# Performance work log

Hardware: AMD Instinct MI355X
Metric: run time of the kernel (lower is better)

Reference implementation:

```python
import jax, jax.numpy as jnp
import numpy as np
from jax import lax

B, T, D, H, C, FF, NH = 256, 48, 89, 128, 64, 64, 8
HD = C // NH


def _pos_encoding(n, c):
    pos = jnp.arange(n, dtype=jnp.float32)[:, None]
    div = jnp.exp(jnp.arange(0, c, 2, dtype=jnp.float32) * (-np.log(10000.0) / c))
    pe = jnp.zeros((n, c), dtype=jnp.float32)
    pe = pe.at[:, 0::2].set(jnp.sin(pos * div))
    pe = pe.at[:, 1::2].set(jnp.cos(pos * div))
    return pe


def _ln(x, g, b):
    m = x.mean(-1, keepdims=True)
    v = ((x - m) ** 2).mean(-1, keepdims=True)
    return (x - m) / jnp.sqrt(v + 1e-5) * g + b


def setup_inputs():
    key = jax.random.key(0)
    ks = iter(jax.random.split(key, 64))
    def n(shape, s=0.05):
        return (jax.random.normal(next(ks), shape) * s).astype(jnp.float32)
    x = jax.random.normal(next(ks), (B, T, D), dtype=jnp.float32)
    mask = (jax.random.uniform(next(ks), (B, T, D)) < 0.8).astype(jnp.float32)
    deltas = (jax.random.uniform(next(ks), (B, T, D)) * 5.0).astype(jnp.float32)
    last_obs = jax.random.normal(next(ks), (B, T, D), dtype=jnp.float32)
    medians = (jax.random.uniform(next(ks), (D,)) * 2.0).astype(jnp.float32)
    return dict(
        x=x, mask=mask, deltas=deltas, last_obs=last_obs, medians=medians,
        W_dh=n((H, D)), b_dh=n((H,)), W_dx=n((D, D)), b_dx=n((D,)),
        W_hist=n((D, H)), b_hist=n((D,)), W_feat=n((D, D)), b_feat=n((D,)),
        W_wc=n((D, 2 * D)), b_wc=n((D,)), W_wo=n((D, D)), b_wo=n((D,)),
        W_cls=n((1, H)), b_cls=n((1,)),
        W_ih=n((3 * H, 2 * D)), W_hh=n((3 * H, H)), b_ih=n((3 * H,)), b_hh=n((3 * H,)),
        W_inp=n((C, D)), b_inp=n((C,)), W_op1=n((H, C)), b_op1=n((H,)),
        W_op2=n((2 * T,)), b_op2=n((1,)),
        attn_in_w=n((3 * C, C)), attn_in_b=n((3 * C,)),
        attn_out_w=n((C, C)), attn_out_b=n((C,)),
        ln1_g=jnp.ones((C,)), ln1_b=jnp.zeros((C,)),
        ln2_g=jnp.ones((C,)), ln2_b=jnp.zeros((C,)),
        ff1_w=n((FF, C)), ff1_b=n((FF,)), ff2_w=n((C, FF)), ff2_b=n((C,)))


def _forward(x, mask, deltas, last_obs, medians,
             W_dh, b_dh, W_dx, b_dx, W_hist, b_hist, W_feat, b_feat,
             W_wc, b_wc, W_wo, b_wo, W_cls, b_cls,
             W_ih, W_hh, b_ih, b_hh, W_inp, b_inp, W_op1, b_op1, W_op2, b_op2,
             attn_in_w, attn_in_b, attn_out_w, attn_out_b,
             ln1_g, ln1_b, ln2_g, ln2_b, ff1_w, ff1_b, ff2_w, ff2_b):
    # Decay_obs: weight = 0.5*(1 - tanh(sign(dd)*|linear(dd)|))
    dd = deltas - medians[None, None, :]
    wd = dd @ W_wo.T + b_wo
    decay_factor = 0.5 * (1.0 - jnp.tanh(jnp.sign(dd) * jnp.abs(wd)))

    # time encoder: 1x1 conv projection + positional encoding
    pe = _pos_encoding(T, C)[None]                      # [1,T,C]
    d_lo = last_obs @ W_inp.T + b_inp + pe              # [B,T,C]
    d_df = decay_factor @ W_inp.T + b_inp + pe          # [B,T,C]
    data = jnp.concatenate([d_lo, d_df], axis=1)        # [B,2T,C]

    # torch TransformerEncoderLayer (post-norm, gelu, dropout off).
    # NOTE: layer is NOT batch_first, so attention runs over axis 0 (B);
    # axis 1 (2T) behaves as the batch — faithful to the source.
    qkv = data @ attn_in_w.T + attn_in_b                # [B,2T,3C]
    q, k, v = jnp.split(qkv, 3, axis=-1)
    q = q.reshape(B, 2 * T, NH, HD)
    k = k.reshape(B, 2 * T, NH, HD)
    v = v.reshape(B, 2 * T, NH, HD)
    scores = jnp.einsum('snhd,tnhd->nhst', q, k) / np.sqrt(HD)
    probs = jax.nn.softmax(scores, axis=-1)
    o = jnp.einsum('nhst,tnhd->snhd', probs, v).reshape(B, 2 * T, C)
    o = o @ attn_out_w.T + attn_out_b
    x1 = _ln(data + o, ln1_g, ln1_b)
    ff = jax.nn.gelu(x1 @ ff1_w.T + ff1_b, approximate=False) @ ff2_w.T + ff2_b
    data = _ln(x1 + ff, ln2_g, ln2_b)                   # [B,2T,C]

    data = data @ W_op1.T + b_op1                       # [B,2T,H]
    h0 = jnp.einsum('bnh,n->bh', data, W_op2) + b_op2[0]  # Conv1d(2T->1,k=1)

    diag_w = jnp.diagonal(W_dx)                         # temp_decay_x diag mask
    offdiag = 1.0 - jnp.eye(D, dtype=x.dtype)

    def step(carry, inp):
        h, loss = carry
        x_t, m_t, d_t = inp
        gamma_h = jnp.exp(-jax.nn.relu(d_t @ W_dh.T + b_dh))
        h = h * gamma_h
        x_h = h @ W_hist.T + b_hist
        x_r = m_t * x_t + (1.0 - m_t) * x_h
        xu = x_r @ (W_feat * offdiag).T + b_feat
        gamma_x = jnp.exp(-jax.nn.relu(d_t * diag_w + b_dx))
        beta = jnp.concatenate([gamma_x, m_t], axis=-1) @ W_wc.T + b_wc
        x_comb = beta * xu + (1.0 - beta) * x_h
        loss = loss + jnp.sum(jnp.abs(x_t - x_comb) * m_t) / (jnp.sum(m_t) + 1e-5)
        x_imp_t = m_t * x_t + (1.0 - m_t) * x_comb
        gi = jnp.concatenate([x_imp_t, m_t], axis=-1) @ W_ih.T + b_ih
        gh = h @ W_hh.T + b_hh
        ir, iz, ig = jnp.split(gi, 3, axis=-1)
        hr, hz, hg = jnp.split(gh, 3, axis=-1)
        r = jax.nn.sigmoid(ir + hr)
        z = jax.nn.sigmoid(iz + hz)
        g = jnp.tanh(ig + r * hg)
        h = (1.0 - z) * g + z * h
        return (h, loss), (x_imp_t, h)

    xs = (x.transpose(1, 0, 2), mask.transpose(1, 0, 2), deltas.transpose(1, 0, 2))
    (h, x_loss), (x_imp_T, hid_T) = lax.scan(step, (h0, jnp.zeros((), x.dtype)), xs)
    x_imp = x_imp_T.transpose(1, 0, 2)                  # [B,T,D]
    hiddens = hid_T.transpose(1, 0, 2)                  # [B,T,H]

    y_out = h @ W_cls.T + b_cls
    y_score = jax.nn.sigmoid(y_out)
    return x_imp, x_loss, hiddens, y_out, y_score


def reference(x, mask, deltas, last_obs, medians,
              W_dh, b_dh, W_dx, b_dx, W_hist, b_hist, W_feat, b_feat,
              W_wc, b_wc, W_wo, b_wo, W_cls, b_cls,
              W_ih, W_hh, b_ih, b_hh, W_inp, b_inp, W_op1, b_op1, W_op2, b_op2,
              attn_in_w, attn_in_b, attn_out_w, attn_out_b,
              ln1_g, ln1_b, ln2_g, ln2_b, ff1_w, ff1_b, ff2_w, ff2_b):
    return _forward(x, mask, deltas, last_obs, medians,
                    W_dh, b_dh, W_dx, b_dx, W_hist, b_hist, W_feat, b_feat,
                    W_wc, b_wc, W_wo, b_wo, W_cls, b_cls,
                    W_ih, W_hh, b_ih, b_hh, W_inp, b_inp, W_op1, b_op1, W_op2, b_op2,
                    attn_in_w, attn_in_b, attn_out_w, attn_out_b,
                    ln1_g, ln1_b, ln2_g, ln2_b, ff1_w, ff1_b, ff2_w, ff2_b)
```

## Files before the change

kernel.cpp:

```cpp
#include <hip/hip_runtime.h>
#include <math.h>

#define B_  256
#define T_  48
#define D_  89
#define H_  128
#define C_  64
#define NH_ 8
#define HD_ 8
#define N2T 96

#define XIMP_OFF 0
#define LOSS_OFF 1093632
#define HID_OFF  1093633
#define Y_OFF    2666497
#define YS_OFF   2666753

typedef unsigned int uint_t;
typedef _Float16 h2_t __attribute__((ext_vector_type(2)));

__device__ __forceinline__ float wave_sum64(float v) {
    v += __shfl_xor(v, 32);
    v += __shfl_xor(v, 16);
    v += __shfl_xor(v, 8);
    v += __shfl_xor(v, 4);
    v += __shfl_xor(v, 2);
    v += __shfl_xor(v, 1);
    return v;
}

__device__ __forceinline__ uint_t packh2(float lo, float hi) {
    union { h2_t h; uint_t u; } c;
    c.h.x = (_Float16)lo;
    c.h.y = (_Float16)hi;
    return c.u;
}
__device__ __forceinline__ h2_t as_h2(uint_t u) {
    union { uint_t u; h2_t h; } c;
    c.u = u;
    return c.h;
}
__device__ __forceinline__ float dot2(uint_t w, float ax, float ay, float acc) {
#if __has_builtin(__builtin_amdgcn_fdot2) && __has_builtin(__builtin_amdgcn_cvt_pkrtz)
    return __builtin_amdgcn_fdot2(as_h2(w), __builtin_amdgcn_cvt_pkrtz(ax, ay), acc, false);
#else
    h2_t h = as_h2(w);
    return fmaf((float)h.y, ay, fmaf((float)h.x, ax, acc));
#endif
}
__device__ __forceinline__ float sigm(float v) { return 1.f / (1.f + __expf(-v)); }

#define DOT96(W, A, acc) do { \
    _Pragma("unroll") \
    for (int it_ = 0; it_ < 3; ++it_) { \
        int idx_ = jj + 8 * it_; \
        uint2 w_ = ((const uint2*)(W))[idx_]; \
        float4 a_ = *(const float4*)((A) + 4 * idx_); \
        acc = dot2(w_.x, a_.x, a_.y, acc); \
        acc = dot2(w_.y, a_.z, a_.w, acc); \
    } } while (0)

#define DOT128(W, A, acc) do { \
    _Pragma("unroll") \
    for (int it_ = 0; it_ < 4; ++it_) { \
        int idx_ = jj + 8 * it_; \
        uint2 w_ = ((const uint2*)(W))[idx_]; \
        float4 a_ = *(const float4*)((A) + 4 * idx_); \
        acc = dot2(w_.x, a_.x, a_.y, acc); \
        acc = dot2(w_.y, a_.z, a_.w, acc); \
    } } while (0)

__device__ __forceinline__ void tr_f32(const float* __restrict__ s, float* __restrict__ d,
                                       int li, int R, int C) {
    int r = li / C, c = li - r * C;
    d[c * R + r] = s[li];
}

__global__ void k_prep(const float* W_wo, const float* W_inp, const float* ain_w,
                       const float* aout_w, const float* ff1_w, const float* ff2_w,
                       const float* W_op1,
                       float* W_woT, float* W_inpT, float* ain_T,
                       float* aout_T, float* ff1_T, float* ff2_T, float* op1_T) {
    int i = blockIdx.x * 256 + threadIdx.x;
    if (i < 7921)         tr_f32(W_wo,   W_woT,  i,          89, 89);
    else if (i < 13617)   tr_f32(W_inp,  W_inpT, i - 7921,   64, 89);
    else if (i < 25905)   tr_f32(ain_w,  ain_T,  i - 13617, 192, 64);
    else if (i < 30001)   tr_f32(aout_w, aout_T, i - 25905,  64, 64);
    else if (i < 34097)   tr_f32(ff1_w,  ff1_T,  i - 30001,  64, 64);
    else if (i < 38193)   tr_f32(ff2_w,  ff2_T,  i - 34097,  64, 64);
    else if (i < 46385)   tr_f32(W_op1,  op1_T,  i - 38193, 128, 64);
}

__global__ void k_pack(const float* __restrict__ W_dh, const float* __restrict__ W_hist,
                       const float* __restrict__ W_ih, const float* __restrict__ W_hh,
                       uint_t* __restrict__ wdh_h, uint_t* __restrict__ whist_h,
                       uint_t* __restrict__ wihx_h, uint_t* __restrict__ wihm_h,
                       uint_t* __restrict__ whh_h) {
    int i = blockIdx.x * 256 + threadIdx.x;
    if (i < 6144) {
        int r = i / 48, c = i - r * 48;
        const float* src = W_dh + r * 89;
        float lo = (c < 45) ? src[2 * c] : 0.f;
        float hi = (c < 44) ? src[2 * c + 1] : 0.f;
        wdh_h[i] = packh2(lo, hi);
    } else if (i < 11840) {
        int j = i - 6144;
        int r = j / 64, c = j - r * 64;
        const float* src = W_hist + r * 128;
        whist_h[j] = packh2(src[2 * c], src[2 * c + 1]);
    } else if (i < 30272) {
        int j = i - 11840;
        int r = j / 48, c = j - r * 48;
        const float* src = W_ih + (size_t)r * 178;
        float lo = (c < 45) ? src[2 * c] : 0.f;
        float hi = (c < 44) ? src[2 * c + 1] : 0.f;
        wihx_h[j] = packh2(lo, hi);
    } else if (i < 48704) {
        int j = i - 30272;
        int r = j / 48, c = j - r * 48;
        const float* src = W_ih + (size_t)r * 178 + 89;
        float lo = (c < 45) ? src[2 * c] : 0.f;
        float hi = (c < 44) ? src[2 * c + 1] : 0.f;
        wihm_h[j] = packh2(lo, hi);
    } else if (i < 73280) {
        int j = i - 48704;
        int r = j / 64, c = j - r * 64;
        const float* src = W_hh + (size_t)r * 128;
        whh_h[j] = packh2(src[2 * c], src[2 * c + 1]);
    }
}

__global__ void k_phaseA(const float* __restrict__ last_obs,
                         const float* __restrict__ deltas,
                         const float* __restrict__ medians,
                         const float* __restrict__ W_woT, const float* __restrict__ b_wo,
                         const float* __restrict__ W_inpT, const float* __restrict__ b_inp,
                         float* __restrict__ data) {
    int bt = blockIdx.x;
    int b = bt / T_;
    int t = bt - b * T_;
    __shared__ float dd[D_], lo[D_], dec[D_];
    int tid = threadIdx.x;
    int base = (b * T_ + t) * D_;
    if (tid < D_) {
        float dv = deltas[base + tid] - medians[tid];
        dd[tid] = dv;
        lo[tid] = last_obs[base + tid];
    }
    __syncthreads();
    if (tid < D_) {
        float acc = b_wo[tid];
        for (int j = 0; j < D_; ++j) acc = fmaf(dd[j], W_woT[j * D_ + tid], acc);
        float dv = dd[tid];
        float s = (dv > 0.f) ? 1.f : ((dv < 0.f) ? -1.f : 0.f);
        dec[tid] = 0.5f * (1.f - tanhf(s * fabsf(acc)));
    }
    __syncthreads();
    int c = tid & 63;
    int half = tid >> 6;
    const float* src = half ? dec : lo;
    float acc = b_inp[c];
    for (int j = 0; j < D_; ++j) acc = fmaf(src[j], W_inpT[j * C_ + c], acc);
    int i = c >> 1;
    float div = __expf((float)i * -0.28782313662425574f);
    float ang = (float)t * div;
    float pe = (c & 1) ? cosf(ang) : sinf(ang);
    data[((b * N2T) + half * T_ + t) * C_ + c] = acc + pe;
}

__global__ void k_qkv(const float* __restrict__ data,
                      const float* __restrict__ ain_T, const float* __restrict__ ain_b,
                      float* __restrict__ qb, float* __restrict__ kb, float* __restrict__ vb) {
    int bn = blockIdx.x;
    int s = bn / N2T;
    int n = bn - s * N2T;
    __shared__ float row[C_];
    int tid = threadIdx.x;
    if (tid < C_) row[tid] = data[bn * C_ + tid];
    __syncthreads();
    float acc = ain_b[tid];
    for (int j = 0; j < C_; ++j) acc = fmaf(row[j], ain_T[j * 192 + tid], acc);
    int part = tid >> 6;
    int c = tid & 63;
    int h = c >> 3, d = c & 7;
    float* dst = (part == 0) ? qb : ((part == 1) ? kb : vb);
    dst[(((n * NH_ + h) * B_ + s) * HD_) + d] = acc;
}

__global__ void k_attn(const float* __restrict__ qb, const float* __restrict__ kb,
                       const float* __restrict__ vb, float* __restrict__ attnO) {
    int n = blockIdx.x >> 3;
    int h = blockIdx.x & 7;
    __shared__ float k_lds[B_][HD_ + 1];
    __shared__ float v_lds[B_][HD_ + 1];
    int s = threadIdx.x;
    const float scale = 0.35355339059327373f;
    size_t base = ((size_t)blockIdx.x * B_ + s) * HD_;
    float q[HD_];
    #pragma unroll
    for (int d = 0; d < HD_; ++d) q[d] = qb[base + d] * scale;
    #pragma unroll
    for (int d = 0; d < HD_; ++d) { k_lds[s][d] = kb[base + d]; v_lds[s][d] = vb[base + d]; }
    __syncthreads();
    float m = -1e30f;
    for (int t = 0; t < B_; ++t) {
        float sc = 0.f;
        #pragma unroll
        for (int d = 0; d < HD_; ++d) sc = fmaf(q[d], k_lds[t][d], sc);
        m = fmaxf(m, sc);
    }
    float l = 0.f;
    float acc[HD_] = {0.f, 0.f, 0.f, 0.f, 0.f, 0.f, 0.f, 0.f};
    for (int t = 0; t < B_; ++t) {
        float sc = 0.f;
        #pragma unroll
        for (int d = 0; d < HD_; ++d) sc = fmaf(q[d], k_lds[t][d], sc);
        float p = __expf(sc - m);
        l += p;
        #pragma unroll
        for (int d = 0; d < HD_; ++d) acc[d] = fmaf(p, v_lds[t][d], acc[d]);
    }
    float inv = 1.f / l;
    float* op = attnO + ((size_t)s * N2T + n) * C_ + h * HD_;
    #pragma unroll
    for (int d = 0; d < HD_; ++d) op[d] = acc[d] * inv;
}

__global__ void k_transform(const float* __restrict__ data,
                            const float* __restrict__ attnO,
                            const float* __restrict__ aout_T, const float* __restrict__ aout_b,
                            const float* __restrict__ ln1_g, const float* __restrict__ ln1_b,
                            const float* __restrict__ ff1_T, const float* __restrict__ ff1_b,
                            const float* __restrict__ ff2_T, const float* __restrict__ ff2_b,
                            const float* __restrict__ ln2_g, const float* __restrict__ ln2_b,
                            const float* __restrict__ op1_T, const float* __restrict__ b_op1,
                            float* __restrict__ val) {
    int bn = blockIdx.x;
    __shared__ float orow[C_], x1s[C_], hbuf[C_], x2s[C_];
    int c = threadIdx.x;
    float d0 = data[bn * C_ + c];
    orow[c] = attnO[bn * C_ + c];
    __syncthreads();
    float acc = aout_b[c];
    for (int j = 0; j < C_; ++j) acc = fmaf(orow[j], aout_T[j * C_ + c], acc);
    float r = d0 + acc;
    float mean = wave_sum64(r) * (1.f / 64.f);
    float df = r - mean;
    float var = wave_sum64(df * df) * (1.f / 64.f);
    float x1 = df * rsqrtf(var + 1e-5f) * ln1_g[c] + ln1_b[c];
    x1s[c] = x1;
    __syncthreads();
    acc = ff1_b[c];
    for (int j = 0; j < C_; ++j) acc = fmaf(x1s[j], ff1_T[j * C_ + c], acc);
    float ge = 0.5f * acc * (1.f + erff(acc * 0.7071067811865475f));
    hbuf[c] = ge;
    __syncthreads();
    acc = ff2_b[c];
    for (int j = 0; j < C_; ++j) acc = fmaf(hbuf[j], ff2_T[j * C_ + c], acc);
    float r2 = x1 + acc;
    float mean2 = wave_sum64(r2) * (1.f / 64.f);
    float df2 = r2 - mean2;
    float var2 = wave_sum64(df2 * df2) * (1.f / 64.f);
    float x2 = df2 * rsqrtf(var2 + 1e-5f) * ln2_g[c] + ln2_b[c];
    x2s[c] = x2;
    __syncthreads();
    #pragma unroll
    for (int rep = 0; rep < 2; ++rep) {
        int k = c + rep * 64;
        float a2 = b_op1[k];
        for (int j = 0; j < C_; ++j) a2 = fmaf(x2s[j], op1_T[j * H_ + k], a2);
        val[(size_t)bn * H_ + k] = a2;
    }
}

__global__ void k_reduce_h0(const float* __restrict__ val,
                            const float* __restrict__ W_op2, const float* __restrict__ b_op2,
                            float* __restrict__ h0) {
    int b = blockIdx.x;
    int h = threadIdx.x;
    float acc = b_op2[0];
    for (int n = 0; n < N2T; ++n)
        acc = fmaf(val[((size_t)b * N2T + n) * H_ + h], W_op2[n], acc);
    h0[b * H_ + h] = acc;
}

__global__ void k_den(const float* __restrict__ mask, float* __restrict__ den) {
    int t = blockIdx.x;
    int tid = threadIdx.x;
    float s = 0.f;
    const int total = B_ * D_;
    for (int i = tid; i < total; i += 256) {
        int b = i / D_;
        int d = i - b * D_;
        s += mask[(b * T_ + t) * D_ + d];
    }
    s = wave_sum64(s);
    __shared__ float red[4];
    if ((tid & 63) == 0) red[tid >> 6] = s;
    __syncthreads();
    if (tid == 0) den[t] = red[0] + red[1] + red[2] + red[3];
}

__global__ __launch_bounds__(1024)
void k_scan(const float* __restrict__ x, const float* __restrict__ mask,
            const float* __restrict__ deltas,
            const uint_t* __restrict__ wdh_h, const float* __restrict__ b_dh,
            const float* __restrict__ W_dx, const float* __restrict__ b_dx,
            const uint_t* __restrict__ whist_h, const float* __restrict__ b_hist,
            const float* __restrict__ W_feat, const float* __restrict__ b_feat,
            const float* __restrict__ W_wc, const float* __restrict__ b_wc,
            const uint_t* __restrict__ wihx_h, const uint_t* __restrict__ wihm_h,
            const uint_t* __restrict__ whh_h,
            const float* __restrict__ b_ih, const float* __restrict__ b_hh,
            const float* __restrict__ W_cls, const float* __restrict__ b_cls,
            const float* __restrict__ h0,
            float* __restrict__ out, float* __restrict__ num_part) {
    int b = blockIdx.x;
    int tid = threadIdx.x;
    int wave = tid >> 6;
    int lane = tid & 63;
    int oo = lane >> 3;
    int jj = lane & 7;

    __shared__ __align__(16) float h_s[H_];
    __shared__ __align__(16) float xt_s[96], dt_s[96], xr_s[96], xh_s[96];
    __shared__ __align__(16) float m_s[96], gx_s[96], ximp_s[96], beta_s[96], diff_s[96];
    __shared__ __align__(16) float gis[384], ghs[384];
    __shared__ __align__(16) uint_t wwcg_l[89 * 48];
    __shared__ __align__(16) uint_t wwcm_l[89 * 48];
    __shared__ __align__(16) uint_t wfeat_l[89 * 48];

    float dxw = 0.f, dxb = 0.f;
    if (tid >= 320 && tid < 409) {
        int o = tid - 320;
        dxw = W_dx[o * 90];
        dxb = b_dx[o];
    }

    for (int i = tid; i < 89 * 48; i += 1024) {
        int r = i / 48, c = i - r * 48;
        const float* wr = W_wc + (size_t)r * 178;
        float lo = (c < 45) ? wr[2 * c] : 0.f;
        float hi = (c < 44) ? wr[2 * c + 1] : 0.f;
        wwcg_l[i] = packh2(lo, hi);
        const float* wm = wr + 89;
        float lo2 = (c < 45) ? wm[2 * c] : 0.f;
        float hi2 = (c < 44) ? wm[2 * c + 1] : 0.f;
        wwcm_l[i] = packh2(lo2, hi2);
        const float* wf = W_feat + r * 89;
        float lo3 = (c < 45 && 2 * c != r) ? wf[2 * c] : 0.f;
        float hi3 = (c < 44 && 2 * c + 1 != r) ? wf[2 * c + 1] : 0.f;
        wfeat_l[i] = packh2(lo3, hi3);
    }
    if (tid < 128) h_s[tid] = h0[b * H_ + tid];
    if (tid >= 416 && tid < 423) {
        int l = tid - 416;
        dt_s[89 + l] = 0.f; xr_s[89 + l] = 0.f; m_s[89 + l] = 0.f;
        gx_s[89 + l] = 0.f; ximp_s[89 + l] = 0.f;
    }
    {
        int base = b * T_ * D_;
        if (tid >= 128 && tid < 217) xt_s[tid - 128] = x[base + tid - 128];
        else if (tid >= 224 && tid < 313) m_s[tid - 224] = mask[base + tid - 224];
        else if (tid >= 320 && tid < 409) {
            int o = tid - 320;
            float dv = deltas[base + o];
            dt_s[o] = dv;
            gx_s[o] = __expf(-fmaxf(dv * dxw + dxb, 0.f));
        }
    }
    __syncthreads();

    for (int t = 0; t < T_; ++t) {
        for (int c = wave; c < 76; c += 16) {
            if (c < 16) {
                int o = c * 8 + oo;
                float acc = 0.f;
                DOT96(wdh_h + o * 48, dt_s, acc);
                acc += __shfl_xor(acc, 1); acc += __shfl_xor(acc, 2); acc += __shfl_xor(acc, 4);
                if (jj == 0) h_s[o] *= __expf(-fmaxf(acc + b_dh[o], 0.f));
            } else if (c < 28) {
                int o = (c - 16) * 8 + oo;
                int ro = (o < 89) ? o : 88;
                float acc = 0.f;
                DOT96(wwcg_l + ro * 48, gx_s, acc);
                DOT96(wwcm_l + ro * 48, m_s, acc);
                acc += __shfl_xor(acc, 1); acc += __shfl_xor(acc, 2); acc += __shfl_xor(acc, 4);
                if (jj == 0 && o < 89) beta_s[o] = acc + b_wc[o];
            } else {
                int o = (c - 28) * 8 + oo;
                float acc = 0.f;
                DOT96(wihm_h + o * 48, m_s, acc);
                acc += __shfl_xor(acc, 1); acc += __shfl_xor(acc, 2); acc += __shfl_xor(acc, 4);
                if (jj == 0) gis[o] = acc + b_ih[o];
            }
        }
        __syncthreads();
        for (int c = wave; c < 60; c += 16) {
            if (c < 12) {
                int o = c * 8 + oo;
                int ro = (o < 89) ? o : 88;
                float acc = 0.f;
                DOT128(whist_h + ro * 64, h_s, acc);
                acc += __shfl_xor(acc, 1); acc += __shfl_xor(acc, 2); acc += __shfl_xor(acc, 4);
                if (jj == 0 && o < 89) {
                    float xh = acc + b_hist[o];
                    xh_s[o] = xh;
                    float m = m_s[o];
                    xr_s[o] = m * xt_s[o] + (1.f - m) * xh;
                }
            } else {
                int o = (c - 12) * 8 + oo;
                float acc = 0.f;
                DOT128(whh_h + o * 64, h_s, acc);
                acc += __shfl_xor(acc, 1); acc += __shfl_xor(acc, 2); acc += __shfl_xor(acc, 4);
                if (jj == 0) ghs[o] = acc + b_hh[o];
            }
        }
        __syncthreads();
        for (int c = wave; c < 12; c += 16) {
            int o = c * 8 + oo;
            int ro = (o < 89) ? o : 88;
            float xu = 0.f;
            DOT96(wfeat_l + ro * 48, xr_s, xu);
            xu += __shfl_xor(xu, 1); xu += __shfl_xor(xu, 2); xu += __shfl_xor(xu, 4);
            if (jj == 0 && o < 89) {
                float xuf = xu + b_feat[o];
                float btf = beta_s[o];
                float xc = btf * xuf + (1.f - btf) * xh_s[o];
                float m = m_s[o];
                float xtv = xt_s[o];
                float xi = m * xtv + (1.f - m) * xc;
                ximp_s[o] = xi;
                out[XIMP_OFF + (b * T_ + t) * D_ + o] = xi;
                diff_s[o] = fabsf(xtv - xc) * m;
            }
        }
        __syncthreads();
        for (int c = wave; c < 48; c += 16) {
            int o = c * 8 + oo;
            float acc = 0.f;
            DOT96(wihx_h + o * 48, ximp_s, acc);
            acc += __shfl_xor(acc, 1); acc += __shfl_xor(acc, 2); acc += __shfl_xor(acc, 4);
            if (jj == 0) gis[o] += acc;
        }
        __syncthreads();
        if (tid < 128) {
            float r = sigm(gis[tid] + ghs[tid]);
            float z = sigm(gis[128 + tid] + ghs[128 + tid]);
            float g = tanhf(gis[256 + tid] + r * ghs[256 + tid]);
            float hn = (1.f - z) * g + z * h_s[tid];
            h_s[tid] = hn;
            out[HID_OFF + (size_t)(b * T_ + t) * H_ + tid] = hn;
        } else if (tid >= 960) {
            int l = tid - 960;
            float s = diff_s[l] + ((l < 25) ? diff_s[64 + l] : 0.f);
            s = wave_sum64(s);
            if (l == 0) num_part[t * B_ + b] = s;
        } else if (t + 1 < T_) {
            int nb = (b * T_ + t + 1) * D_;
            if (tid < 217) xt_s[tid - 128] = x[nb + tid - 128];
            else if (tid >= 224 && tid < 313) m_s[tid - 224] = mask[nb + tid - 224];
            else if (tid >= 320 && tid < 409) {
                int o = tid - 320;
                float dv = deltas[nb + o];
                dt_s[o] = dv;
                gx_s[o] = __expf(-fmaxf(dv * dxw + dxb, 0.f));
            }
        }
        __syncthreads();
    }
    if (tid < 64) {
        float p = h_s[tid] * W_cls[tid] + h_s[tid + 64] * W_cls[tid + 64];
        p = wave_sum64(p);
        if (tid == 0) {
            float y = p + b_cls[0];
            out[Y_OFF + b] = y;
            out[YS_OFF + b] = 1.f / (1.f + __expf(-y));
        }
    }
}

__global__ void k_loss(const float* __restrict__ num_part, const float* __restrict__ den,
                       float* __restrict__ out) {
    int tid = threadIdx.x;
    float v = 0.f;
    if (tid < T_) {
        float s = 0.f;
        const float* np_ = num_part + tid * B_;
        for (int b = 0; b < B_; ++b) s += np_[b];
        v = s / (den[tid] + 1e-5f);
    }
    v = wave_sum64(v);
    if (tid == 0) out[LOSS_OFF] = v;
}

extern "C" void kernel_launch(void* const* d_in, const int* in_sizes, int n_in,
                              void* d_out, int out_size, void* d_ws, size_t ws_size,
                              hipStream_t stream) {
    const float* x        = (const float*)d_in[0];
    const float* mask     = (const float*)d_in[1];
    const float* deltas   = (const float*)d_in[2];
    const float* last_obs = (const float*)d_in[3];
    const float* medians  = (const float*)d_in[4];
    const float* W_dh  = (const float*)d_in[5];
    const float* b_dh  = (const float*)d_in[6];
    const float* W_dx  = (const float*)d_in[7];
    const float* b_dx  = (const float*)d_in[8];
    const float* W_hist= (const float*)d_in[9];
    const float* b_hist= (const float*)d_in[10];
    const float* W_feat= (const float*)d_in[11];
    const float* b_feat= (const float*)d_in[12];
    const float* W_wc  = (const float*)d_in[13];
    const float* b_wc  = (const float*)d_in[14];
    const float* W_wo  = (const float*)d_in[15];
    const float* b_wo  = (const float*)d_in[16];
    const float* W_cls = (const float*)d_in[17];
    const float* b_cls = (const float*)d_in[18];
    const float* W_ih  = (const float*)d_in[19];
    const float* W_hh  = (const float*)d_in[20];
    const float* b_ih  = (const float*)d_in[21];
    const float* b_hh  = (const float*)d_in[22];
    const float* W_inp = (const float*)d_in[23];
    const float* b_inp = (const float*)d_in[24];
    const float* W_op1 = (const float*)d_in[25];
    const float* b_op1 = (const float*)d_in[26];
    const float* W_op2 = (const float*)d_in[27];
    const float* b_op2 = (const float*)d_in[28];
    const float* attn_in_w  = (const float*)d_in[29];
    const float* attn_in_b  = (const float*)d_in[30];
    const float* attn_out_w = (const float*)d_in[31];
    const float* attn_out_b = (const float*)d_in[32];
    const float* ln1_g = (const float*)d_in[33];
    const float* ln1_b = (const float*)d_in[34];
    const float* ln2_g = (const float*)d_in[35];
    const float* ln2_b = (const float*)d_in[36];
    const float* ff1_w = (const float*)d_in[37];
    const float* ff1_b = (const float*)d_in[38];
    const float* ff2_w = (const float*)d_in[39];
    const float* ff2_b = (const float*)d_in[40];

    float* out = (float*)d_out;
    float* ws = (float*)d_ws;

    float* data  = ws;
    float* qb    = data  + (size_t)B_ * N2T * C_;
    float* kb    = qb    + (size_t)N2T * NH_ * B_ * HD_;
    float* vb    = kb    + (size_t)N2T * NH_ * B_ * HD_;
    float* attnO = vb    + (size_t)N2T * NH_ * B_ * HD_;
    float* val   = attnO + (size_t)B_ * N2T * C_;
    float* h0    = val   + (size_t)B_ * N2T * H_;
    float* den   = h0    + (size_t)B_ * H_;
    float* nump  = den   + 64;
    float* W_woT = nump  + T_ * B_;
    float* W_inpT= W_woT + 7921;
    float* ain_T = W_inpT + 5696;
    float* aout_T= ain_T + 12288;
    float* ff1_T = aout_T + 4096;
    float* ff2_T = ff1_T + 4096;
    float* op1_T = ff2_T + 4096;
    uint_t* wdh_h   = (uint_t*)(op1_T + 8192);
    uint_t* whist_h = wdh_h + 6144;
    uint_t* wihx_h  = whist_h + 5696;
    uint_t* wihm_h  = wihx_h + 18432;
    uint_t* whh_h   = wihm_h + 18432;

    k_prep<<<182, 256, 0, stream>>>(W_wo, W_inp, attn_in_w, attn_out_w, ff1_w, ff2_w, W_op1,
                                    W_woT, W_inpT, ain_T, aout_T, ff1_T, ff2_T, op1_T);
    k_pack<<<287, 256, 0, stream>>>(W_dh, W_hist, W_ih, W_hh,
                                    wdh_h, whist_h, wihx_h, wihm_h, whh_h);
    k_phaseA<<<B_ * T_, 128, 0, stream>>>(last_obs, deltas, medians, W_woT, b_wo, W_inpT, b_inp, data);
    k_qkv<<<B_ * N2T, 192, 0, stream>>>(data, ain_T, attn_in_b, qb, kb, vb);
    k_attn<<<N2T * NH_, 256, 0, stream>>>(qb, kb, vb, attnO);
    k_transform<<<B_ * N2T, 64, 0, stream>>>(data, attnO, aout_T, attn_out_b,
                                             ln1_g, ln1_b, ff1_T, ff1_b, ff2_T, ff2_b,
                                             ln2_g, ln2_b, op1_T, b_op1, val);
    k_reduce_h0<<<B_, H_, 0, stream>>>(val, W_op2, b_op2, h0);
    k_den<<<T_, 256, 0, stream>>>(mask, den);
    k_scan<<<B_, 1024, 0, stream>>>(x, mask, deltas,
                                    wdh_h, b_dh, W_dx, b_dx, whist_h, b_hist, W_feat, b_feat,
                                    W_wc, b_wc, wihx_h, wihm_h, whh_h, b_ih, b_hh, W_cls, b_cls,
                                    h0, out, nump);
    k_loss<<<1, 64, 0, stream>>>(nump, den, out);
}
```

Measured before the change: 591.8 us.

## Fuse QKV into attention, merge weight prep kernels, pack scan activations to fp16

```diff
diff --git a/kernel.cpp b/kernel.cpp
--- a/kernel.cpp
+++ b/kernel.cpp
@@ -40,34 +40,34 @@
     c.u = u;
     return c.h;
 }
-__device__ __forceinline__ float dot2(uint_t w, float ax, float ay, float acc) {
-#if __has_builtin(__builtin_amdgcn_fdot2) && __has_builtin(__builtin_amdgcn_cvt_pkrtz)
-    return __builtin_amdgcn_fdot2(as_h2(w), __builtin_amdgcn_cvt_pkrtz(ax, ay), acc, false);
+__device__ __forceinline__ float dot2h(uint_t w, uint_t a, float acc) {
+#if __has_builtin(__builtin_amdgcn_fdot2)
+    return __builtin_amdgcn_fdot2(as_h2(w), as_h2(a), acc, false);
 #else
-    h2_t h = as_h2(w);
-    return fmaf((float)h.y, ay, fmaf((float)h.x, ax, acc));
+    h2_t hw = as_h2(w), ha = as_h2(a);
+    return fmaf((float)hw.y, (float)ha.y, fmaf((float)hw.x, (float)ha.x, acc));
 #endif
 }
 __device__ __forceinline__ float sigm(float v) { return 1.f / (1.f + __expf(-v)); }
 
-#define DOT96(W, A, acc) do { \
+#define DOT96H(W, A, acc) do { \
     _Pragma("unroll") \
     for (int it_ = 0; it_ < 3; ++it_) { \
         int idx_ = jj + 8 * it_; \
         uint2 w_ = ((const uint2*)(W))[idx_]; \
-        float4 a_ = *(const float4*)((A) + 4 * idx_); \
-        acc = dot2(w_.x, a_.x, a_.y, acc); \
-        acc = dot2(w_.y, a_.z, a_.w, acc); \
+        uint2 a_ = ((const uint2*)(A))[idx_]; \
+        acc = dot2h(w_.x, a_.x, acc); \
+        acc = dot2h(w_.y, a_.y, acc); \
     } } while (0)
 
-#define DOT128(W, A, acc) do { \
+#define DOT128H(W, A, acc) do { \
     _Pragma("unroll") \
     for (int it_ = 0; it_ < 4; ++it_) { \
         int idx_ = jj + 8 * it_; \
         uint2 w_ = ((const uint2*)(W))[idx_]; \
-        float4 a_ = *(const float4*)((A) + 4 * idx_); \
-        acc = dot2(w_.x, a_.x, a_.y, acc); \
-        acc = dot2(w_.y, a_.z, a_.w, acc); \
+        uint2 a_ = ((const uint2*)(A))[idx_]; \
+        acc = dot2h(w_.x, a_.x, acc); \
+        acc = dot2h(w_.y, a_.y, acc); \
     } } while (0)
 
 __device__ __forceinline__ void tr_f32(const float* __restrict__ s, float* __restrict__ d,
@@ -76,11 +76,16 @@
     d[c * R + r] = s[li];
 }
 
-__global__ void k_prep(const float* W_wo, const float* W_inp, const float* ain_w,
-                       const float* aout_w, const float* ff1_w, const float* ff2_w,
-                       const float* W_op1,
-                       float* W_woT, float* W_inpT, float* ain_T,
-                       float* aout_T, float* ff1_T, float* ff2_T, float* op1_T) {
+__global__ void k_wprep(const float* W_wo, const float* W_inp, const float* ain_w,
+                        const float* aout_w, const float* ff1_w, const float* ff2_w,
+                        const float* W_op1,
+                        float* W_woT, float* W_inpT, float* ain_T,
+                        float* aout_T, float* ff1_T, float* ff2_T, float* op1_T,
+                        const float* __restrict__ W_dh, const float* __restrict__ W_hist,
+                        const float* __restrict__ W_ih, const float* __restrict__ W_hh,
+                        uint_t* __restrict__ wdh_h, uint_t* __restrict__ whist_h,
+                        uint_t* __restrict__ wihx_h, uint_t* __restrict__ wihm_h,
+                        uint_t* __restrict__ whh_h) {
     int i = blockIdx.x * 256 + threadIdx.x;
     if (i < 7921)         tr_f32(W_wo,   W_woT,  i,          89, 89);
     else if (i < 13617)   tr_f32(W_inp,  W_inpT, i - 7921,   64, 89);
@@ -89,44 +94,39 @@
     else if (i < 34097)   tr_f32(ff1_w,  ff1_T,  i - 30001,  64, 64);
     else if (i < 38193)   tr_f32(ff2_w,  ff2_T,  i - 34097,  64, 64);
     else if (i < 46385)   tr_f32(W_op1,  op1_T,  i - 38193, 128, 64);
-}
-
-__global__ void k_pack(const float* __restrict__ W_dh, const float* __restrict__ W_hist,
-                       const float* __restrict__ W_ih, const float* __restrict__ W_hh,
-                       uint_t* __restrict__ wdh_h, uint_t* __restrict__ whist_h,
-                       uint_t* __restrict__ wihx_h, uint_t* __restrict__ wihm_h,
-                       uint_t* __restrict__ whh_h) {
-    int i = blockIdx.x * 256 + threadIdx.x;
-    if (i < 6144) {
-        int r = i / 48, c = i - r * 48;
-        const float* src = W_dh + r * 89;
-        float lo = (c < 45) ? src[2 * c] : 0.f;
-        float hi = (c < 44) ? src[2 * c + 1] : 0.f;
-        wdh_h[i] = packh2(lo, hi);
-    } else if (i < 11840) {
-        int j = i - 6144;
-        int r = j / 64, c = j - r * 64;
-        const float* src = W_hist + r * 128;
-        whist_h[j] = packh2(src[2 * c], src[2 * c + 1]);
-    } else if (i < 30272) {
-        int j = i - 11840;
-        int r = j / 48, c = j - r * 48;
-        const float* src = W_ih + (size_t)r * 178;
-        float lo = (c < 45) ? src[2 * c] : 0.f;
-        float hi = (c < 44) ? src[2 * c + 1] : 0.f;
-        wihx_h[j] = packh2(lo, hi);
-    } else if (i < 48704) {
-        int j = i - 30272;
-        int r = j / 48, c = j - r * 48;
-        const float* src = W_ih + (size_t)r * 178 + 89;
-        float lo = (c < 45) ? src[2 * c] : 0.f;
-        float hi = (c < 44) ? src[2 * c + 1] : 0.f;
-        wihm_h[j] = packh2(lo, hi);
-    } else if (i < 73280) {
-        int j = i - 48704;
-        int r = j / 64, c = j - r * 64;
-        const float* src = W_hh + (size_t)r * 128;
-        whh_h[j] = packh2(src[2 * c], src[2 * c + 1]);
+    else {
+        int p = i - 46385;
+        if (p < 6144) {
+            int r = p / 48, c = p - r * 48;
+            const float* src = W_dh + r * 89;
+            float lo = (c < 45) ? src[2 * c] : 0.f;
+            float hi = (c < 44) ? src[2 * c + 1] : 0.f;
+            wdh_h[p] = packh2(lo, hi);
+        } else if (p < 11840) {
+            int j = p - 6144;
+            int r = j / 64, c = j - r * 64;
+            const float* src = W_hist + r * 128;
+            whist_h[j] = packh2(src[2 * c], src[2 * c + 1]);
+        } else if (p < 30272) {
+            int j = p - 11840;
+            int r = j / 48, c = j - r * 48;
+            const float* src = W_ih + (size_t)r * 178;
+            float lo = (c < 45) ? src[2 * c] : 0.f;
+            float hi = (c < 44) ? src[2 * c + 1] : 0.f;
+            wihx_h[j] = packh2(lo, hi);
+        } else if (p < 48704) {
+            int j = p - 30272;
+            int r = j / 48, c = j - r * 48;
+            const float* src = W_ih + (size_t)r * 178 + 89;
+            float lo = (c < 45) ? src[2 * c] : 0.f;
+            float hi = (c < 44) ? src[2 * c + 1] : 0.f;
+            wihm_h[j] = packh2(lo, hi);
+        } else if (p < 73280) {
+            int j = p - 48704;
+            int r = j / 64, c = j - r * 64;
+            const float* src = W_hh + (size_t)r * 128;
+            whh_h[j] = packh2(src[2 * c], src[2 * c + 1]);
+        }
     }
 }
 
@@ -168,60 +168,66 @@
     data[((b * N2T) + half * T_ + t) * C_ + c] = acc + pe;
 }
 
-__global__ void k_qkv(const float* __restrict__ data,
-                      const float* __restrict__ ain_T, const float* __restrict__ ain_b,
-                      float* __restrict__ qb, float* __restrict__ kb, float* __restrict__ vb) {
-    int bn = blockIdx.x;
-    int s = bn / N2T;
-    int n = bn - s * N2T;
-    __shared__ float row[C_];
-    int tid = threadIdx.x;
-    if (tid < C_) row[tid] = data[bn * C_ + tid];
-    __syncthreads();
-    float acc = ain_b[tid];
-    for (int j = 0; j < C_; ++j) acc = fmaf(row[j], ain_T[j * 192 + tid], acc);
-    int part = tid >> 6;
-    int c = tid & 63;
-    int h = c >> 3, d = c & 7;
-    float* dst = (part == 0) ? qb : ((part == 1) ? kb : vb);
-    dst[(((n * NH_ + h) * B_ + s) * HD_) + d] = acc;
-}
-
-__global__ void k_attn(const float* __restrict__ qb, const float* __restrict__ kb,
-                       const float* __restrict__ vb, float* __restrict__ attnO) {
+__global__ __launch_bounds__(256)
+void k_attn(const float* __restrict__ data,
+            const float* __restrict__ ain_T, const float* __restrict__ ain_b,
+            float* __restrict__ attnO) {
     int n = blockIdx.x >> 3;
     int h = blockIdx.x & 7;
-    __shared__ float k_lds[B_][HD_ + 1];
-    __shared__ float v_lds[B_][HD_ + 1];
-    int s = threadIdx.x;
+    int tid = threadIdx.x;
+    __shared__ float stage[64][65];
+    __shared__ float q_l[B_][HD_ + 1];
+    __shared__ float k_l[B_][HD_ + 1];
+    __shared__ float v_l[B_][HD_ + 1];
     const float scale = 0.35355339059327373f;
-    size_t base = ((size_t)blockIdx.x * B_ + s) * HD_;
+    int col_b = h * 8;
+    for (int tt = 0; tt < 4; ++tt) {
+        #pragma unroll
+        for (int l = 0; l < 16; ++l) {
+            int flat = l * 256 + tid;
+            int r = flat >> 6, c2 = flat & 63;
+            stage[r][c2] = data[((size_t)((tt * 64 + r) * N2T + n)) * C_ + c2];
+        }
+        __syncthreads();
+        #pragma unroll
+        for (int it = 0; it < 6; ++it) {
+            int oi = it * 256 + tid;
+            int r = oi / 24, comp = oi - r * 24;
+            int part = comp >> 3, d = comp & 7;
+            int col = part * 64 + col_b + d;
+            float acc = ain_b[col];
+            for (int j = 0; j < 64; ++j) acc = fmaf(stage[r][j], ain_T[j * 192 + col], acc);
+            int s2 = tt * 64 + r;
+            if (part == 0) q_l[s2][d] = acc * scale;
+            else if (part == 1) k_l[s2][d] = acc;
+            else v_l[s2][d] = acc;
+        }
+        __syncthreads();
+    }
+    int s = tid;
     float q[HD_];
     #pragma unroll
-    for (int d = 0; d < HD_; ++d) q[d] = qb[base + d] * scale;
-    #pragma unroll
-    for (int d = 0; d < HD_; ++d) { k_lds[s][d] = kb[base + d]; v_lds[s][d] = vb[base + d]; }
-    __syncthreads();
-    float m = -1e30f;
+    for (int d = 0; d < HD_; ++d) q[d] = q_l[s][d];
+    float mx = -1e30f;
     for (int t = 0; t < B_; ++t) {
         float sc = 0.f;
         #pragma unroll
-        for (int d = 0; d < HD_; ++d) sc = fmaf(q[d], k_lds[t][d], sc);
-        m = fmaxf(m, sc);
+        for (int d = 0; d < HD_; ++d) sc = fmaf(q[d], k_l[t][d], sc);
+        mx = fmaxf(mx, sc);
     }
     float l = 0.f;
     float acc[HD_] = {0.f, 0.f, 0.f, 0.f, 0.f, 0.f, 0.f, 0.f};
     for (int t = 0; t < B_; ++t) {
         float sc = 0.f;
         #pragma unroll
-        for (int d = 0; d < HD_; ++d) sc = fmaf(q[d], k_lds[t][d], sc);
-        float p = __expf(sc - m);
+        for (int d = 0; d < HD_; ++d) sc = fmaf(q[d], k_l[t][d], sc);
+        float p = __expf(sc - mx);
         l += p;
         #pragma unroll
-        for (int d = 0; d < HD_; ++d) acc[d] = fmaf(p, v_lds[t][d], acc[d]);
+        for (int d = 0; d < HD_; ++d) acc[d] = fmaf(p, v_l[t][d], acc[d]);
     }
     float inv = 1.f / l;
-    float* op = attnO + ((size_t)s * N2T + n) * C_ + h * HD_;
+    float* op = attnO + ((size_t)s * N2T + n) * C_ + col_b;
     #pragma unroll
     for (int d = 0; d < HD_; ++d) op[d] = acc[d] * inv;
 }
@@ -323,16 +329,17 @@
     int jj = lane & 7;
 
     __shared__ __align__(16) float h_s[H_];
-    __shared__ __align__(16) float xt_s[96], dt_s[96], xr_s[96], xh_s[96];
-    __shared__ __align__(16) float m_s[96], gx_s[96], ximp_s[96], beta_s[96], diff_s[96];
+    __shared__ __align__(16) uint_t h_h[64];
+    __shared__ __align__(16) float xt_s[96], m_s[96], xh_s[96], beta_s[96], diff_s[96];
+    __shared__ __align__(16) uint_t dt_h[48], gx_h[48], m_h[48], xr_h[48], ximp_h[48];
     __shared__ __align__(16) float gis[384], ghs[384];
     __shared__ __align__(16) uint_t wwcg_l[89 * 48];
     __shared__ __align__(16) uint_t wwcm_l[89 * 48];
     __shared__ __align__(16) uint_t wfeat_l[89 * 48];
 
     float dxw = 0.f, dxb = 0.f;
-    if (tid >= 320 && tid < 409) {
-        int o = tid - 320;
+    if (tid >= 384 && tid < 473) {
+        int o = tid - 384;
         dxw = W_dx[o * 90];
         dxb = b_dx[o];
     }
@@ -352,21 +359,36 @@
         float hi3 = (c < 44 && 2 * c + 1 != r) ? wf[2 * c + 1] : 0.f;
         wfeat_l[i] = packh2(lo3, hi3);
     }
-    if (tid < 128) h_s[tid] = h0[b * H_ + tid];
-    if (tid >= 416 && tid < 423) {
-        int l = tid - 416;
-        dt_s[89 + l] = 0.f; xr_s[89 + l] = 0.f; m_s[89 + l] = 0.f;
-        gx_s[89 + l] = 0.f; ximp_s[89 + l] = 0.f;
+    if (tid < 128) {
+        float hv = h0[b * H_ + tid];
+        h_s[tid] = hv;
+        float nx = __shfl_down(hv, 1);
+        if ((tid & 1) == 0) h_h[tid >> 1] = packh2(hv, nx);
+    }
+    if (tid == 500) {
+        #pragma unroll
+        for (int k = 45; k < 48; ++k) {
+            dt_h[k] = 0u; gx_h[k] = 0u; m_h[k] = 0u; xr_h[k] = 0u; ximp_h[k] = 0u;
+        }
     }
     {
-        int base = b * T_ * D_;
-        if (tid >= 128 && tid < 217) xt_s[tid - 128] = x[base + tid - 128];
-        else if (tid >= 224 && tid < 313) m_s[tid - 224] = mask[base + tid - 224];
-        else if (tid >= 320 && tid < 409) {
-            int o = tid - 320;
-            float dv = deltas[base + o];
-            dt_s[o] = dv;
-            gx_s[o] = __expf(-fmaxf(dv * dxw + dxb, 0.f));
+        int nb = b * T_ * D_;
+        if (tid >= 128 && tid < 217) xt_s[tid - 128] = x[nb + tid - 128];
+        else if (tid >= 256 && tid < 345) {
+            int o = tid - 256;
+            float mv = mask[nb + o];
+            m_s[o] = mv;
+            float nx = __shfl_down(mv, 1);
+            if (o + 1 >= 89) nx = 0.f;
+            if ((o & 1) == 0) m_h[o >> 1] = packh2(mv, nx);
+        } else if (tid >= 384 && tid < 473) {
+            int o = tid - 384;
+            float dv = deltas[nb + o];
+            float gxv = __expf(-fmaxf(dv * dxw + dxb, 0.f));
+            float nd = __shfl_down(dv, 1);
+            float ng = __shfl_down(gxv, 1);
+            if (o + 1 >= 89) { nd = 0.f; ng = 0.f; }
+            if ((o & 1) == 0) { dt_h[o >> 1] = packh2(dv, nd); gx_h[o >> 1] = packh2(gxv, ng); }
         }
     }
     __syncthreads();
@@ -376,21 +398,26 @@
             if (c < 16) {
                 int o = c * 8 + oo;
                 float acc = 0.f;
-                DOT96(wdh_h + o * 48, dt_s, acc);
+                DOT96H(wdh_h + o * 48, dt_h, acc);
                 acc += __shfl_xor(acc, 1); acc += __shfl_xor(acc, 2); acc += __shfl_xor(acc, 4);
-                if (jj == 0) h_s[o] *= __expf(-fmaxf(acc + b_dh[o], 0.f));
+                if (jj == 0) {
+                    float hv = h_s[o] * __expf(-fmaxf(acc + b_dh[o], 0.f));
+                    h_s[o] = hv;
+                    float nx = __shfl_down(hv, 8);
+                    if ((oo & 1) == 0) h_h[o >> 1] = packh2(hv, nx);
+                }
             } else if (c < 28) {
                 int o = (c - 16) * 8 + oo;
                 int ro = (o < 89) ? o : 88;
                 float acc = 0.f;
-                DOT96(wwcg_l + ro * 48, gx_s, acc);
-                DOT96(wwcm_l + ro * 48, m_s, acc);
+                DOT96H(wwcg_l + ro * 48, gx_h, acc);
+                DOT96H(wwcm_l + ro * 48, m_h, acc);
                 acc += __shfl_xor(acc, 1); acc += __shfl_xor(acc, 2); acc += __shfl_xor(acc, 4);
                 if (jj == 0 && o < 89) beta_s[o] = acc + b_wc[o];
             } else {
                 int o = (c - 28) * 8 + oo;
                 float acc = 0.f;
-                DOT96(wihm_h + o * 48, m_s, acc);
+                DOT96H(wihm_h + o * 48, m_h, acc);
                 acc += __shfl_xor(acc, 1); acc += __shfl_xor(acc, 2); acc += __shfl_xor(acc, 4);
                 if (jj == 0) gis[o] = acc + b_ih[o];
             }
@@ -401,18 +428,21 @@
                 int o = c * 8 + oo;
                 int ro = (o < 89) ? o : 88;
                 float acc = 0.f;
-                DOT128(whist_h + ro * 64, h_s, acc);
+                DOT128H(whist_h + ro * 64, h_h, acc);
                 acc += __shfl_xor(acc, 1); acc += __shfl_xor(acc, 2); acc += __shfl_xor(acc, 4);
-                if (jj == 0 && o < 89) {
-                    float xh = acc + b_hist[o];
-                    xh_s[o] = xh;
-                    float m = m_s[o];
-                    xr_s[o] = m * xt_s[o] + (1.f - m) * xh;
+                if (jj == 0) {
+                    float xh = acc + b_hist[ro];
+                    float m = m_s[ro];
+                    float xrv = m * xt_s[ro] + (1.f - m) * xh;
+                    float nx = __shfl_down(xrv, 8);
+                    if (o + 1 >= 89) nx = 0.f;
+                    if (o < 89) xh_s[o] = xh;
+                    if ((oo & 1) == 0 && o < 89) xr_h[o >> 1] = packh2(xrv, nx);
                 }
             } else {
                 int o = (c - 12) * 8 + oo;
                 float acc = 0.f;
-                DOT128(whh_h + o * 64, h_s, acc);
+                DOT128H(whh_h + o * 64, h_h, acc);
                 acc += __shfl_xor(acc, 1); acc += __shfl_xor(acc, 2); acc += __shfl_xor(acc, 4);
                 if (jj == 0) ghs[o] = acc + b_hh[o];
             }
@@ -422,25 +452,29 @@
             int o = c * 8 + oo;
             int ro = (o < 89) ? o : 88;
             float xu = 0.f;
-            DOT96(wfeat_l + ro * 48, xr_s, xu);
+            DOT96H(wfeat_l + ro * 48, xr_h, xu);
             xu += __shfl_xor(xu, 1); xu += __shfl_xor(xu, 2); xu += __shfl_xor(xu, 4);
-            if (jj == 0 && o < 89) {
-                float xuf = xu + b_feat[o];
-                float btf = beta_s[o];
-                float xc = btf * xuf + (1.f - btf) * xh_s[o];
-                float m = m_s[o];
-                float xtv = xt_s[o];
+            if (jj == 0) {
+                float xuf = xu + b_feat[ro];
+                float btf = beta_s[ro];
+                float xc = btf * xuf + (1.f - btf) * xh_s[ro];
+                float m = m_s[ro];
+                float xtv = xt_s[ro];
                 float xi = m * xtv + (1.f - m) * xc;
-                ximp_s[o] = xi;
-                out[XIMP_OFF + (b * T_ + t) * D_ + o] = xi;
-                diff_s[o] = fabsf(xtv - xc) * m;
+                float nx = __shfl_down(xi, 8);
+                if (o + 1 >= 89) nx = 0.f;
+                if (o < 89) {
+                    out[XIMP_OFF + (b * T_ + t) * D_ + o] = xi;
+                    diff_s[o] = fabsf(xtv - xc) * m;
+                }
+                if ((oo & 1) == 0 && o < 89) ximp_h[o >> 1] = packh2(xi, nx);
             }
         }
         __syncthreads();
         for (int c = wave; c < 48; c += 16) {
             int o = c * 8 + oo;
             float acc = 0.f;
-            DOT96(wihx_h + o * 48, ximp_s, acc);
+            DOT96H(wihx_h + o * 48, ximp_h, acc);
             acc += __shfl_xor(acc, 1); acc += __shfl_xor(acc, 2); acc += __shfl_xor(acc, 4);
             if (jj == 0) gis[o] += acc;
         }
@@ -452,6 +486,8 @@
             float hn = (1.f - z) * g + z * h_s[tid];
             h_s[tid] = hn;
             out[HID_OFF + (size_t)(b * T_ + t) * H_ + tid] = hn;
+            float nx = __shfl_down(hn, 1);
+            if ((tid & 1) == 0) h_h[tid >> 1] = packh2(hn, nx);
         } else if (tid >= 960) {
             int l = tid - 960;
             float s = diff_s[l] + ((l < 25) ? diff_s[64 + l] : 0.f);
@@ -460,12 +496,21 @@
         } else if (t + 1 < T_) {
             int nb = (b * T_ + t + 1) * D_;
             if (tid < 217) xt_s[tid - 128] = x[nb + tid - 128];
-            else if (tid >= 224 && tid < 313) m_s[tid - 224] = mask[nb + tid - 224];
-            else if (tid >= 320 && tid < 409) {
-                int o = tid - 320;
+            else if (tid >= 256 && tid < 345) {
+                int o = tid - 256;
+                float mv = mask[nb + o];
+                m_s[o] = mv;
+                float nx = __shfl_down(mv, 1);
+                if (o + 1 >= 89) nx = 0.f;
+                if ((o & 1) == 0) m_h[o >> 1] = packh2(mv, nx);
+            } else if (tid >= 384 && tid < 473) {
+                int o = tid - 384;
                 float dv = deltas[nb + o];
-                dt_s[o] = dv;
-                gx_s[o] = __expf(-fmaxf(dv * dxw + dxb, 0.f));
+                float gxv = __expf(-fmaxf(dv * dxw + dxb, 0.f));
+                float nd = __shfl_down(dv, 1);
+                float ng = __shfl_down(gxv, 1);
+                if (o + 1 >= 89) { nd = 0.f; ng = 0.f; }
+                if ((o & 1) == 0) { dt_h[o >> 1] = packh2(dv, nd); gx_h[o >> 1] = packh2(gxv, ng); }
             }
         }
         __syncthreads();
@@ -544,10 +589,7 @@
     float* ws = (float*)d_ws;
 
     float* data  = ws;
-    float* qb    = data  + (size_t)B_ * N2T * C_;
-    float* kb    = qb    + (size_t)N2T * NH_ * B_ * HD_;
-    float* vb    = kb    + (size_t)N2T * NH_ * B_ * HD_;
-    float* attnO = vb    + (size_t)N2T * NH_ * B_ * HD_;
+    float* attnO = data  + (size_t)B_ * N2T * C_;
     float* val   = attnO + (size_t)B_ * N2T * C_;
     float* h0    = val   + (size_t)B_ * N2T * H_;
     float* den   = h0    + (size_t)B_ * H_;
@@ -565,13 +607,12 @@
     uint_t* wihm_h  = wihx_h + 18432;
     uint_t* whh_h   = wihm_h + 18432;
 
-    k_prep<<<182, 256, 0, stream>>>(W_wo, W_inp, attn_in_w, attn_out_w, ff1_w, ff2_w, W_op1,
-                                    W_woT, W_inpT, ain_T, aout_T, ff1_T, ff2_T, op1_T);
-    k_pack<<<287, 256, 0, stream>>>(W_dh, W_hist, W_ih, W_hh,
-                                    wdh_h, whist_h, wihx_h, wihm_h, whh_h);
+    k_wprep<<<468, 256, 0, stream>>>(W_wo, W_inp, attn_in_w, attn_out_w, ff1_w, ff2_w, W_op1,
+                                     W_woT, W_inpT, ain_T, aout_T, ff1_T, ff2_T, op1_T,
+                                     W_dh, W_hist, W_ih, W_hh,
+                                     wdh_h, whist_h, wihx_h, wihm_h, whh_h);
     k_phaseA<<<B_ * T_, 128, 0, stream>>>(last_obs, deltas, medians, W_woT, b_wo, W_inpT, b_inp, data);
-    k_qkv<<<B_ * N2T, 192, 0, stream>>>(data, ain_T, attn_in_b, qb, kb, vb);
-    k_attn<<<N2T * NH_, 256, 0, stream>>>(qb, kb, vb, attnO);
+    k_attn<<<N2T * NH_, 256, 0, stream>>>(data, ain_T, attn_in_b, attnO);
     k_transform<<<B_ * N2T, 64, 0, stream>>>(data, attnO, aout_T, attn_out_b,
                                              ln1_g, ln1_b, ff1_T, ff1_b, ff2_T, ff2_b,
                                              ln2_g, ln2_b, op1_T, b_op1, val);
```

Measured after the change: 750.7 us. 1.27x slower.
